# Optimization experiments

Measured on AMD Instinct MI355X. Metric: run time of the kernel, lower is better.

Reference implementation:

```python
import jax, jax.numpy as jnp
import numpy as np

B, S, NB = 8, 512, 23
INIT, E, R, T = 512, 256, 3, 2
NEG = -9e8

def _gru(x, h, wih, whh, bih, bhh):
    gi = x @ wih.T + bih
    gh = h @ whh.T + bhh
    ir, iz, inn = jnp.split(gi, 3, axis=-1)
    hr, hz, hn = jnp.split(gh, 3, axis=-1)
    r = jax.nn.sigmoid(ir + hr)
    z = jax.nn.sigmoid(iz + hz)
    n = jnp.tanh(inn + r * hn)
    return (1.0 - z) * n + z * h

def setup_inputs():
    key = jax.random.key(0)
    ks = jax.random.split(key, 30)
    def lin(k, o, i):
        return jax.random.normal(k, (o, i), jnp.float32) * 0.02
    def vec(k, n):
        return jax.random.normal(k, (n,), jnp.float32) * 0.02
    inp = {}
    inp["amino_list"] = jax.random.normal(ks[0], (B, S, INIT), jnp.float32)
    inp["amino_mask"] = (jax.random.uniform(ks[1], (B, S)) < 0.9).astype(jnp.float32)
    inp["emb_W"] = lin(ks[2], E, INIT); inp["emb_b"] = vec(ks[3], E)
    inp["nb_W"] = lin(ks[4], E, INIT); inp["nb_b"] = vec(ks[5], E)
    inp["align_W"] = jax.random.normal(ks[6], (R, 1, 2 * E), jnp.float32) * 0.02
    inp["align_b"] = jax.random.normal(ks[7], (R, 1), jnp.float32) * 0.02
    inp["attend_W"] = jax.random.normal(ks[8], (R, E, E), jnp.float32) * 0.02
    inp["attend_b"] = jax.random.normal(ks[9], (R, E), jnp.float32) * 0.02
    inp["gru_wih"] = jax.random.normal(ks[10], (R, 3 * E, E), jnp.float32) * 0.02
    inp["gru_whh"] = jax.random.normal(ks[11], (R, 3 * E, E), jnp.float32) * 0.02
    inp["gru_bih"] = jax.random.normal(ks[12], (R, 3 * E), jnp.float32) * 0.02
    inp["gru_bhh"] = jax.random.normal(ks[13], (R, 3 * E), jnp.float32) * 0.02
    inp["seq_align_W"] = lin(ks[14], 1, 2 * E); inp["seq_align_b"] = vec(ks[15], 1)
    inp["seq_attend_W"] = lin(ks[16], E, E); inp["seq_attend_b"] = vec(ks[17], E)
    inp["seq_gru_wih"] = lin(ks[18], 3 * E, E); inp["seq_gru_bih"] = vec(ks[19], 3 * E)
    inp["seq_gru_whh"] = lin(ks[20], 3 * E, E); inp["seq_gru_bhh"] = vec(ks[21], 3 * E)
    inp["amino_degree_list"] = jax.random.randint(ks[22], (B, S, NB), -1, S)
    return inp

def reference(amino_list, amino_mask, emb_W, emb_b, nb_W, nb_b, align_W, align_b,
              attend_W, attend_b, gru_wih, gru_whh, gru_bih, gru_bhh,
              seq_align_W, seq_align_b, seq_attend_W, seq_attend_b,
              seq_gru_wih, seq_gru_whh, seq_gru_bih, seq_gru_bhh, amino_degree_list):
    idx = amino_degree_list
    lrelu = jax.nn.leaky_relu
    # per-batch neighbor gather: (S,D),(S,NB) -> (S,NB,D); index -1 wraps (masked out below)
    gather = jax.vmap(lambda f, i: f[i])
    feat = lrelu(amino_list @ emb_W.T + emb_b)               # (B,S,E)
    nfeat = lrelu(gather(amino_list, idx) @ nb_W.T + nb_b)   # (B,S,NB,E)
    attend_mask = (idx != -1).astype(feat.dtype)             # (B,S,NB)
    smask = jnp.where(idx == -1, NEG, 0.0).astype(feat.dtype)

    def attn(d, center, nbr):
        # align Linear on concat([center, nbr]) split into two matvecs (same math, no concat)
        aW = align_W[d, 0]
        score = lrelu(jnp.einsum('bse,e->bs', center, aW[:E])[:, :, None]
                      + jnp.einsum('bsne,e->bsn', nbr, aW[E:]) + align_b[d, 0])
        w = jax.nn.softmax(score + smask, axis=-1) * attend_mask   # softmax over neighbor axis
        nt = nbr @ attend_W[d].T + attend_b[d]
        return jax.nn.elu(jnp.einsum('bsn,bsne->bse', w, nt))

    h = _gru(attn(0, feat, nfeat).reshape(-1, E), feat.reshape(-1, E),
             gru_wih[0], gru_whh[0], gru_bih[0], gru_bhh[0])
    act = jax.nn.relu(h.reshape(B, S, E))
    for d in range(1, R):
        ctx = attn(d, act, gather(act, idx))
        h = _gru(ctx.reshape(-1, E), h, gru_wih[d], gru_whh[d], gru_bih[d], gru_bhh[d])
        act = jax.nn.relu(h.reshape(B, S, E))

    seq_feature = jnp.sum(act * amino_mask[:, :, None], axis=1)  # (B,E)
    act_mol = jax.nn.relu(seq_feature)                           # fixed across T (as in torch)
    seq_smask = jnp.where(amino_mask == 0, NEG, 0.0)
    saW = seq_align_W[0]
    act_seq = act_mol
    for _ in range(T):
        score = lrelu((act_mol @ saW[:E])[:, None]
                      + jnp.einsum('bse,e->bs', act, saW[E:]) + seq_align_b[0])
        w = jax.nn.softmax(score + seq_smask, axis=-1) * amino_mask  # softmax over seq axis
        tf = act @ seq_attend_W.T + seq_attend_b
        seq_ctx = jax.nn.elu(jnp.einsum('bs,bse->be', w, tf))
        seq_feature = _gru(seq_ctx, seq_feature, seq_gru_wih, seq_gru_whh, seq_gru_bih, seq_gru_bhh)
        act_seq = jax.nn.relu(seq_feature)
    return (act_seq, act)
```

## Files before the change

### kernel.cpp

```cpp
#include <hip/hip_runtime.h>
#include <math.h>


#define BSZ   8
#define SEQ   512
#define NBR   23
#define EMB   256
#define INITD 512
#define BS    (BSZ*SEQ)
#define G3    (3*EMB)
#define NEGV  -9e8f

typedef __attribute__((ext_vector_type(8))) short short8;
typedef __attribute__((ext_vector_type(4))) float f32x4;

__device__ __forceinline__ float lrelu(float x){ return x > 0.f ? x : 0.01f*x; }
__device__ __forceinline__ float elu1 (float x){ return x > 0.f ? x : (expf(x)-1.f); }
__device__ __forceinline__ float sigm (float x){ return 1.f/(1.f+expf(-x)); }
__device__ __forceinline__ float bf2f(ushort u){
    union { unsigned int i; float f; } v; v.i = ((unsigned int)u) << 16; return v.f;
}
__device__ __forceinline__ ushort f2bf(float f){
    union { float f; unsigned int i; } v; v.f = f;
    unsigned int u = v.i;
    return (ushort)((u + 0x7FFFu + ((u >> 16) & 1u)) >> 16);
}

__device__ __forceinline__ void gload_lds16(const void* g, void* l) {
    __builtin_amdgcn_global_load_lds(
        (const __attribute__((address_space(1))) unsigned int*)g,
        (__attribute__((address_space(3))) unsigned int*)l,
        16, 0, 0);
}

template<int BN> struct GemmLdsT {
    ushort A[2][128][64];
    ushort B[2][BN][64];
};

__global__ __launch_bounds__(256) void convert9_kernel(
    const float* s0, ushort* d0, int n0,
    const float* s1, ushort* d1, int n1,
    const float* s2, ushort* d2, int n2,
    const float* s3, ushort* d3, int n3,
    const float* s4, ushort* d4, int n4,
    const float* s5, ushort* d5, int n5,
    const float* s6, ushort* d6, int n6,
    const float* s7, ushort* d7, int n7,
    const float* s8, ushort* d8, int n8)
{
    const float* srcs[9] = {s0,s1,s2,s3,s4,s5,s6,s7,s8};
    ushort* dsts[9] = {d0,d1,d2,d3,d4,d5,d6,d7,d8};
    int ns[9] = {n0,n1,n2,n3,n4,n5,n6,n7,n8};
    int seg = blockIdx.y;
    const float* s = srcs[seg]; ushort* d = dsts[seg]; int n = ns[seg];
    size_t i = ((size_t)blockIdx.x * 256 + threadIdx.x) * 8;
    size_t stride = (size_t)gridDim.x * 256 * 8;
    for (; i < (size_t)n; i += stride) {
        float4 a = *reinterpret_cast<const float4*>(s + i);
        float4 b = *reinterpret_cast<const float4*>(s + i + 4);
        uint4 o;
        o.x = (unsigned)f2bf(a.x) | ((unsigned)f2bf(a.y) << 16);
        o.y = (unsigned)f2bf(a.z) | ((unsigned)f2bf(a.w) << 16);
        o.z = (unsigned)f2bf(b.x) | ((unsigned)f2bf(b.y) << 16);
        o.w = (unsigned)f2bf(b.z) | ((unsigned)f2bf(b.w) << 16);
        *reinterpret_cast<uint4*>(d + i) = o;
    }
}

template<int BN, int ACT, bool WF32, bool WBF>
__device__ __forceinline__ void gemm_dev(
    const ushort* __restrict__ A, const ushort* __restrict__ W,
    const float* __restrict__ bias,
    float* __restrict__ C, ushort* __restrict__ Cbf,
    int N, int K, int bx, int by, GemmLdsT<BN>& L)
{
    constexpr int FN = BN / 32;
    const int tid = threadIdx.x;
    const int m0 = bx * 128, n0 = by * BN;
    const int wv = tid >> 6, lane = tid & 63;
    const int fr = lane & 15, grp = lane >> 4;
    const int kc = K >> 3;
    const int mh = wv & 1, nh = wv >> 1;
    const int lrow = lane >> 3;
    const int csrc = (lane & 7) ^ lrow;

    f32x4 acc[4][FN];
    #pragma unroll
    for (int i = 0; i < 4; ++i)
        #pragma unroll
        for (int n = 0; n < FN; ++n) acc[i][n] = (f32x4){0.f,0.f,0.f,0.f};

    auto stage = [&](int c, int k0) {
        const int kch = (k0 >> 3) + csrc;
        #pragma unroll
        for (int i = 0; i < 4; ++i) {
            const int s = (wv << 2) + i;
            const ushort* g = A + ((size_t)(m0 + (s << 3) + lrow) * kc + kch) * 8;
            gload_lds16(g, &L.A[c][s << 3][0]);
        }
        #pragma unroll
        for (int i = 0; i < FN; ++i) {
            const int s = wv * FN + i;
            const ushort* g = W + ((size_t)(n0 + (s << 3) + lrow) * kc + kch) * 8;
            gload_lds16(g, &L.B[c][s << 3][0]);
        }
    };

    auto compute = [&](int c) {
        #pragma unroll
        for (int ks = 0; ks < 2; ++ks) {
            short8 af[4];
            #pragma unroll
            for (int i = 0; i < 4; ++i) {
                const int ar = (mh << 6) + (i << 4) + fr;
                af[i] = *reinterpret_cast<const short8*>(
                    &L.A[c][ar][(((ks << 2) + grp) ^ (ar & 7)) << 3]);
            }
            #pragma unroll
            for (int n = 0; n < FN; ++n) {
                const int br = nh * (BN/2) + (n << 4) + fr;
                short8 bv = *reinterpret_cast<const short8*>(
                    &L.B[c][br][(((ks << 2) + grp) ^ (br & 7)) << 3]);
                #pragma unroll
                for (int i = 0; i < 4; ++i)
                    acc[i][n] = __builtin_amdgcn_mfma_f32_16x16x32_bf16(
                        af[i], bv, acc[i][n], 0, 0, 0);
            }
        }
    };

    const int KT = K >> 6;
    stage(0, 0);
    __syncthreads();
    int cur = 0;
    for (int kt = 1; kt < KT; ++kt) {
        stage(cur ^ 1, kt << 6);
        compute(cur);
        __syncthreads();
        cur ^= 1;
    }
    compute(cur);

    #pragma unroll
    for (int i = 0; i < 4; ++i) {
        const int mrow = m0 + (mh << 6) + (i << 4) + (grp << 2);
        #pragma unroll
        for (int n = 0; n < FN; ++n) {
            const int col = n0 + nh * (BN/2) + (n << 4) + fr;
            const float bv = bias[col];
            #pragma unroll
            for (int j = 0; j < 4; ++j) {
                float t = acc[i][n][j] + bv;
                if (ACT == 1) t = lrelu(t);
                size_t off = (size_t)(mrow + j) * N + col;
                if (WF32) C[off] = t;
                if (WBF)  Cbf[off] = f2bf(t);
            }
        }
    }
}

template<int ACT, bool WF32, bool WBF>
__global__ __launch_bounds__(256) void gemm_mfma128(
    const ushort* __restrict__ A, const ushort* __restrict__ W,
    const float* __restrict__ bias,
    float* __restrict__ C, ushort* __restrict__ Cbf, int N, int K)
{
    __shared__ GemmLdsT<128> L;
    gemm_dev<128,ACT,WF32,WBF>(A, W, bias, C, Cbf, N, K,
                               blockIdx.x & 31, blockIdx.x >> 5, L);
}

__global__ __launch_bounds__(256) void featnbase_kernel(
    const ushort* __restrict__ aminobf,
    const ushort* __restrict__ embWbf, const float* __restrict__ embB,
    float* __restrict__ feat, ushort* __restrict__ featbf,
    const ushort* __restrict__ nbWbf, const float* __restrict__ nbB,
    float* __restrict__ nbase, ushort* __restrict__ nbasebf)
{
    __shared__ GemmLdsT<64> L;
    int blk = blockIdx.x;
    if (blk < 128)
        gemm_dev<64,1,true,true>(aminobf, embWbf, embB, feat, featbf,
                                 EMB, INITD, blk & 31, blk >> 5, L);
    else {
        blk -= 128;
        gemm_dev<64,1,true,true>(aminobf, nbWbf, nbB, nbase, nbasebf,
                                 EMB, INITD, blk & 31, blk >> 5, L);
    }
}

__global__ __launch_bounds__(256) void round_pre_kernel(
    const ushort* __restrict__ nbrbf, const ushort* __restrict__ attWd,
    const float* __restrict__ attBd, ushort* __restrict__ ntb,
    const ushort* __restrict__ hprevbf, const ushort* __restrict__ gwhhd,
    const float* __restrict__ gbhhd, ushort* __restrict__ ghbf,
    const float* __restrict__ center, const float* __restrict__ nbrbase,
    const float* __restrict__ alignWd,
    float* __restrict__ cdot, float* __restrict__ ndot)
{
    __shared__ GemmLdsT<128> L;
    int blk = blockIdx.x;
    if (blk < 64) {
        gemm_dev<128,0,false,true>(nbrbf, attWd, attBd, nullptr, ntb,
                                   EMB, EMB, blk & 31, blk >> 5, L);
    } else if (blk < 256) {
        int b = blk - 64;
        gemm_dev<128,0,false,true>(hprevbf, gwhhd, gbhhd, nullptr, ghbf,
                                   G3, EMB, b & 31, b >> 5, L);
    } else {
        const int b    = blk - 256;
        const int lane = threadIdx.x & 63;
        const int wv   = threadIdx.x >> 6;
        const int e    = lane << 2;
        const int rb   = b * 32 + wv * 8;
        float4 w0 = *reinterpret_cast<const float4*>(&alignWd[e]);
        float4 w1 = *reinterpret_cast<const float4*>(&alignWd[EMB + e]);
        #pragma unroll
        for (int i = 0; i < 8; ++i) {
            const int r = rb + i;
            float4 xc = *reinterpret_cast<const float4*>(&center[(size_t)r*EMB + e]);
            float4 xn = *reinterpret_cast<const float4*>(&nbrbase[(size_t)r*EMB + e]);
            float ac = xc.x*w0.x + xc.y*w0.y + xc.z*w0.z + xc.w*w0.w;
            float an = xn.x*w1.x + xn.y*w1.y + xn.z*w1.z + xn.w*w1.w;
            #pragma unroll
            for (int off = 32; off; off >>= 1) {
                ac += __shfl_xor(ac, off, 64);
                an += __shfl_xor(an, off, 64);
            }
            if (lane == 0) { cdot[r] = ac; ndot[r] = an; }
        }
    }
}

__global__ __launch_bounds__(256) void attn_kernel(
    const float* __restrict__ cdot, const float* __restrict__ ndot,
    const int* __restrict__ idx, const ushort* __restrict__ nt,
    const float* __restrict__ alignB, ushort* __restrict__ ctxbf)
{
    const int lane = threadIdx.x & 63;
    const int r = blockIdx.x * 4 + (threadIdx.x >> 6);
    const int b = r >> 9;
    float sc = -3e38f, vm = 0.f; int row = 0;
    if (lane < NBR) {
        int j = idx[(size_t)r*NBR + lane];
        int valid = (j >= 0);
        int jj = valid ? j : j + SEQ;
        row = b*SEQ + jj;
        vm = (float)valid;
        sc = lrelu(cdot[r] + ndot[row] + alignB[0]) + (valid ? 0.f : NEGV);
    }
    float m = sc;
    #pragma unroll
    for (int off = 32; off; off >>= 1) m = fmaxf(m, __shfl_xor(m, off, 64));
    float ev = (lane < NBR) ? expf(sc - m) : 0.f;
    float s = ev;
    #pragma unroll
    for (int off = 32; off; off >>= 1) s += __shfl_xor(s, off, 64);
    float wgt = ev * vm / s;
    float acc0 = 0.f, acc1 = 0.f, acc2 = 0.f, acc3 = 0.f;
    const int e = lane << 2;
    #pragma unroll 1
    for (int n = 0; n < NBR; ++n) {
        float wn = __shfl(wgt, n, 64);
        int   rn = __shfl(row, n, 64);
        ushort4 v = *reinterpret_cast<const ushort4*>(&nt[(size_t)rn*EMB + e]);
        acc0 += wn * bf2f(v.x); acc1 += wn * bf2f(v.y);
        acc2 += wn * bf2f(v.z); acc3 += wn * bf2f(v.w);
    }
    uint2 o;
    o.x = (unsigned)f2bf(elu1(acc0)) | ((unsigned)f2bf(elu1(acc1)) << 16);
    o.y = (unsigned)f2bf(elu1(acc2)) | ((unsigned)f2bf(elu1(acc3)) << 16);
    *reinterpret_cast<uint2*>(&ctxbf[(size_t)r*EMB + e]) = o;
}

__global__ __launch_bounds__(256) void gru_kernel(
    const ushort* __restrict__ gibf, const ushort* __restrict__ ghbf,
    const float* __restrict__ hprev,
    float* __restrict__ hout, ushort* __restrict__ hbf,
    float* __restrict__ actout, ushort* __restrict__ actbf)
{
    const size_t r = blockIdx.x * 4 + (threadIdx.x >> 6);
    const int    e = (threadIdx.x & 63) << 2;
    const size_t gb = r*G3 + e, hb = r*EMB + e;
    ushort4 ir4 = *reinterpret_cast<const ushort4*>(&gibf[gb]);
    ushort4 iz4 = *reinterpret_cast<const ushort4*>(&gibf[gb + EMB]);
    ushort4 in4 = *reinterpret_cast<const ushort4*>(&gibf[gb + 2*EMB]);
    ushort4 hr4 = *reinterpret_cast<const ushort4*>(&ghbf[gb]);
    ushort4 hz4 = *reinterpret_cast<const ushort4*>(&ghbf[gb + EMB]);
    ushort4 hn4 = *reinterpret_cast<const ushort4*>(&ghbf[gb + 2*EMB]);
    float4 hp4 = *reinterpret_cast<const float4*>(&hprev[hb]);
    const float ir_[4] = {bf2f(ir4.x),bf2f(ir4.y),bf2f(ir4.z),bf2f(ir4.w)};
    const float iz_[4] = {bf2f(iz4.x),bf2f(iz4.y),bf2f(iz4.z),bf2f(iz4.w)};
    const float in_[4] = {bf2f(in4.x),bf2f(in4.y),bf2f(in4.z),bf2f(in4.w)};
    const float hr_[4] = {bf2f(hr4.x),bf2f(hr4.y),bf2f(hr4.z),bf2f(hr4.w)};
    const float hz_[4] = {bf2f(hz4.x),bf2f(hz4.y),bf2f(hz4.z),bf2f(hz4.w)};
    const float hn_[4] = {bf2f(hn4.x),bf2f(hn4.y),bf2f(hn4.z),bf2f(hn4.w)};
    const float hp_[4] = {hp4.x,hp4.y,hp4.z,hp4.w};
    float hv[4], av[4];
    #pragma unroll
    for (int i = 0; i < 4; ++i) {
        float rg = sigm(ir_[i] + hr_[i]);
        float z  = sigm(iz_[i] + hz_[i]);
        float n  = tanhf(in_[i] + rg*hn_[i]);
        hv[i] = (1.f - z)*n + z*hp_[i];
        av[i] = fmaxf(hv[i], 0.f);
    }
    *reinterpret_cast<float4*>(&hout[hb])   = make_float4(hv[0],hv[1],hv[2],hv[3]);
    *reinterpret_cast<float4*>(&actout[hb]) = make_float4(av[0],av[1],av[2],av[3]);
    uint2 hp, ap;
    hp.x = (unsigned)f2bf(hv[0]) | ((unsigned)f2bf(hv[1]) << 16);
    hp.y = (unsigned)f2bf(hv[2]) | ((unsigned)f2bf(hv[3]) << 16);
    ap.x = (unsigned)f2bf(av[0]) | ((unsigned)f2bf(av[1]) << 16);
    ap.y = (unsigned)f2bf(av[2]) | ((unsigned)f2bf(av[3]) << 16);
    *reinterpret_cast<uint2*>(&hbf[hb])   = hp;
    *reinterpret_cast<uint2*>(&actbf[hb]) = ap;
}

__global__ __launch_bounds__(256) void seqpre_kernel(
    const ushort* __restrict__ actbf, const ushort* __restrict__ satWbf,
    const float* __restrict__ satB, float* __restrict__ tf,
    const float* __restrict__ act, const float* __restrict__ mask,
    const float* __restrict__ saW,
    float* __restrict__ seqfeat, float* __restrict__ cmol,
    float* __restrict__ ad)
{
    __shared__ GemmLdsT<64> L;
    int blk = blockIdx.x;
    if (blk < 128) {
        gemm_dev<64,0,true,false>(actbf, satWbf, satB, tf, nullptr,
                                  EMB, EMB, blk & 31, blk >> 5, L);
    } else if (blk < 136) {
        const int b = blk - 128;
        const int e = threadIdx.x;
        float acc = 0.f;
        for (int s = 0; s < SEQ; ++s)
            acc += act[((size_t)b*SEQ + s)*EMB + e] * mask[b*SEQ + s];
        seqfeat[b*EMB + e] = acc;
        float* red = reinterpret_cast<float*>(&L);
        red[e] = fmaxf(acc, 0.f) * saW[e];
        __syncthreads();
        for (int off = 128; off; off >>= 1) {
            if (e < off) red[e] += red[e + off];
            __syncthreads();
        }
        if (e == 0) cmol[b] = red[0];
    } else {
        const int b2   = blk - 136;
        const int lane = threadIdx.x & 63;
        const int wv   = threadIdx.x >> 6;
        const int e    = lane << 2;
        const int rb   = b2 * 32 + wv * 8;
        float4 w1 = *reinterpret_cast<const float4*>(&saW[EMB + e]);
        #pragma unroll
        for (int i = 0; i < 8; ++i) {
            const int r = rb + i;
            float4 xa = *reinterpret_cast<const float4*>(&act[(size_t)r*EMB + e]);
            float an = xa.x*w1.x + xa.y*w1.y + xa.z*w1.z + xa.w*w1.w;
            #pragma unroll
            for (int off = 32; off; off >>= 1) an += __shfl_xor(an, off, 64);
            if (lane == 0) ad[r] = an;
        }
    }
}

__global__ __launch_bounds__(256) void seqpv2_kernel(
    const float* __restrict__ ad, const float* __restrict__ mask,
    const float* __restrict__ saB, const float* __restrict__ cmol,
    const float* __restrict__ tf, float* __restrict__ partial)
{
    const int st = blockIdx.x, b = blockIdx.y;
    const int tid = threadIdx.x;
    __shared__ float w_s[SEQ];
    __shared__ float red[256];
    float mk0 = mask[b*SEQ + tid], mk1 = mask[b*SEQ + 256 + tid];
    float cb = cmol[b], bb = saB[0];
    float s0 = lrelu(cb + ad[b*SEQ + tid] + bb)       + (mk0 == 0.f ? NEGV : 0.f);
    float s1 = lrelu(cb + ad[b*SEQ + 256 + tid] + bb) + (mk1 == 0.f ? NEGV : 0.f);
    red[tid] = fmaxf(s0, s1); __syncthreads();
    for (int off = 128; off; off >>= 1) {
        if (tid < off) red[tid] = fmaxf(red[tid], red[tid + off]);
        __syncthreads();
    }
    float m = red[0]; __syncthreads();
    float e0 = expf(s0 - m), e1 = expf(s1 - m);
    red[tid] = e0 + e1; __syncthreads();
    for (int off = 128; off; off >>= 1) {
        if (tid < off) red[tid] += red[tid + off];
        __syncthreads();
    }
    float inv = 1.f / red[0];
    w_s[tid]       = e0 * inv * mk0;
    w_s[tid + 256] = e1 * inv * mk1;
    __syncthreads();
    float acc = 0.f;
    const int s0i = st * 32;
    #pragma unroll 4
    for (int s = s0i; s < s0i + 32; ++s)
        acc += w_s[s] * tf[((size_t)b*SEQ + s)*EMB + tid];
    partial[((size_t)b*16 + st)*EMB + tid] = acc;
}

template<int T0>
__global__ __launch_bounds__(512) void seqstep_kernel(
    const float* __restrict__ partial, const float* __restrict__ sfin,
    const ushort* __restrict__ sgwihbf, const float* __restrict__ sgbih,
    const ushort* __restrict__ sgwhhbf, const float* __restrict__ sgbhh,
    float* __restrict__ sgi, float* __restrict__ sfout,
    float* __restrict__ actseq)
{
    const int b = blockIdx.x >> 2, q = blockIdx.x & 3;
    const int tid = threadIdx.x, lane = tid & 63, wv = tid >> 6;
    __shared__ float xs[EMB];
    __shared__ float hs[EMB];
    __shared__ float gis[192], ghs[192];
    if (tid < EMB) {
        hs[tid] = sfin[b*EMB + tid];
        if (T0) {
            float a = 0.f;
            #pragma unroll
            for (int st = 0; st < 16; ++st)
                a += partial[((size_t)b*16 + st)*EMB + tid];
            xs[tid] = elu1(a);
        }
    }
    if (!T0) {
        for (int l = tid; l < 192; l += 512) {
            int g = (l >> 6)*EMB + (q << 6) + (l & 63);
            gis[l] = sgi[b*G3 + g];
        }
    }
    __syncthreads();
    const int nrows = T0 ? 384 : 192;
    const int rpw = nrows >> 3;
    for (int i = 0; i < rpw; ++i) {
        const int l = wv * rpw + i;
        const int iswih = T0 && (l < 192);
        const int ll = (T0 && l >= 192) ? l - 192 : l;
        const int g = (ll >> 6)*EMB + (q << 6) + (ll & 63);
        const ushort* Wm = iswih ? sgwihbf : sgwhhbf;
        ushort4 w4 = *reinterpret_cast<const ushort4*>(&Wm[(size_t)g*EMB + (lane << 2)]);
        float4 x4 = *reinterpret_cast<const float4*>(iswih ? &xs[lane << 2] : &hs[lane << 2]);
        float d = bf2f(w4.x)*x4.x + bf2f(w4.y)*x4.y + bf2f(w4.z)*x4.z + bf2f(w4.w)*x4.w;
        #pragma unroll
        for (int off = 32; off; off >>= 1) d += __shfl_xor(d, off, 64);
        if (lane == 0) {
            if (iswih) {
                d += sgbih[g];
                gis[ll] = d;
                sgi[b*G3 + g] = d;
            } else {
                ghs[ll] = d + sgbhh[g];
            }
        }
    }
    __syncthreads();
    if (tid < 64) {
        const int e = (q << 6) + tid;
        float rg = sigm(gis[tid]       + ghs[tid]);
        float z  = sigm(gis[64 + tid]  + ghs[64 + tid]);
        float n  = tanhf(gis[128 + tid] + rg*ghs[128 + tid]);
        float hv = (1.f - z)*n + z*hs[e];
        sfout[b*EMB + e]  = hv;
        actseq[b*EMB + e] = fmaxf(hv, 0.f);
    }
}

extern "C" void kernel_launch(void* const* d_in, const int* in_sizes, int n_in,
                              void* d_out, int out_size, void* d_ws, size_t ws_size,
                              hipStream_t stream) {
    (void)in_sizes; (void)n_in; (void)out_size; (void)ws_size;
    const float* amino  = (const float*)d_in[0];
    const float* mask   = (const float*)d_in[1];
    const float* embW   = (const float*)d_in[2];
    const float* embB   = (const float*)d_in[3];
    const float* nbW    = (const float*)d_in[4];
    const float* nbB    = (const float*)d_in[5];
    const float* alignW = (const float*)d_in[6];
    const float* alignB = (const float*)d_in[7];
    const float* attW   = (const float*)d_in[8];
    const float* attB   = (const float*)d_in[9];
    const float* gwih   = (const float*)d_in[10];
    const float* gwhh   = (const float*)d_in[11];
    const float* gbih   = (const float*)d_in[12];
    const float* gbhh   = (const float*)d_in[13];
    const float* saW    = (const float*)d_in[14];
    const float* saB    = (const float*)d_in[15];
    const float* satW   = (const float*)d_in[16];
    const float* satB   = (const float*)d_in[17];
    const float* sgwih  = (const float*)d_in[18];
    const float* sgbih  = (const float*)d_in[19];
    const float* sgwhh  = (const float*)d_in[20];
    const float* sgbhh  = (const float*)d_in[21];
    const int*   idx    = (const int*)d_in[22];

    char* cur = (char*)d_ws;
    auto alloc = [&](size_t bytes) -> char* {
        char* p = cur; cur += (bytes + 255) & ~(size_t)255; return p;
    };
    float* feat    = (float*)alloc((size_t)BS*EMB*4);
    float* nbase   = (float*)alloc((size_t)BS*EMB*4);
    float* h       = (float*)alloc((size_t)BS*EMB*4);
    float* tf      = (float*)alloc((size_t)BS*EMB*4);
    float* cdot    = (float*)alloc(BS*4);
    float* ndot    = (float*)alloc(BS*4);
    float* ad      = (float*)alloc(BS*4);
    float* seqfeat = (float*)alloc(BSZ*EMB*4);
    float* sf2     = (float*)alloc(BSZ*EMB*4);
    float* cmol    = (float*)alloc(64*4);
    float* sgi     = (float*)alloc(BSZ*G3*4);
    float* partial = (float*)alloc((size_t)BSZ*16*EMB*4);
    ushort* aminobf = (ushort*)alloc((size_t)BS*INITD*2);
    ushort* featbf  = (ushort*)alloc((size_t)BS*EMB*2);
    ushort* nbasebf = (ushort*)alloc((size_t)BS*EMB*2);
    ushort* actbf   = (ushort*)alloc((size_t)BS*EMB*2);
    ushort* hbf     = (ushort*)alloc((size_t)BS*EMB*2);
    ushort* ctxbf   = (ushort*)alloc((size_t)BS*EMB*2);
    ushort* ntb     = (ushort*)alloc((size_t)BS*EMB*2);
    ushort* gibf    = (ushort*)alloc((size_t)BS*G3*2);
    ushort* ghbf    = (ushort*)alloc((size_t)BS*G3*2);
    ushort* embWbf  = (ushort*)alloc((size_t)EMB*INITD*2);
    ushort* nbWbf   = (ushort*)alloc((size_t)EMB*INITD*2);
    ushort* attWbf  = (ushort*)alloc((size_t)3*EMB*EMB*2);
    ushort* gwihbf  = (ushort*)alloc((size_t)3*G3*EMB*2);
    ushort* gwhhbf  = (ushort*)alloc((size_t)3*G3*EMB*2);
    ushort* satWbf  = (ushort*)alloc((size_t)EMB*EMB*2);
    ushort* sgwihbf = (ushort*)alloc((size_t)G3*EMB*2);
    ushort* sgwhhbf = (ushort*)alloc((size_t)G3*EMB*2);

    float* out    = (float*)d_out;
    float* actseq = out;
    float* act    = out + BSZ*EMB;

    convert9_kernel<<<dim3(1024, 9), 256, 0, stream>>>(
        amino, aminobf, BS*INITD,
        embW,  embWbf,  EMB*INITD,
        nbW,   nbWbf,   EMB*INITD,
        attW,  attWbf,  3*EMB*EMB,
        gwih,  gwihbf,  3*G3*EMB,
        gwhh,  gwhhbf,  3*G3*EMB,
        satW,  satWbf,  EMB*EMB,
        sgwih, sgwihbf, G3*EMB,
        sgwhh, sgwhhbf, G3*EMB);

    featnbase_kernel<<<256, 256, 0, stream>>>(
        aminobf, embWbf, embB, feat, featbf, nbWbf, nbB, nbase, nbasebf);

    for (int d = 0; d < 3; ++d) {
        const float*  center   = (d == 0) ? feat    : act;
        const float*  nbrbase  = (d == 0) ? nbase   : act;
        const ushort* nbrbf    = (d == 0) ? nbasebf : actbf;
        const float*  hprev    = (d == 0) ? feat    : h;
        const ushort* hprevbf  = (d == 0) ? featbf  : hbf;
        round_pre_kernel<<<384, 256, 0, stream>>>(
            nbrbf, attWbf + (size_t)d*EMB*EMB, attB + d*EMB, ntb,
            hprevbf, gwhhbf + (size_t)d*G3*EMB, gbhh + d*G3, ghbf,
            center, nbrbase, alignW + d*2*EMB, cdot, ndot);
        attn_kernel<<<BS/4, 256, 0, stream>>>(cdot, ndot, idx, ntb, alignB + d, ctxbf);
        gemm_mfma128<0,false,true><<<192, 256, 0, stream>>>(
            ctxbf, gwihbf + (size_t)d*G3*EMB, gbih + d*G3, nullptr, gibf, G3, EMB);
        gru_kernel<<<BS/4, 256, 0, stream>>>(gibf, ghbf, hprev, h, hbf, act, actbf);
    }

    seqpre_kernel<<<264, 256, 0, stream>>>(
        actbf, satWbf, satB, tf, act, mask, saW, seqfeat, cmol, ad);
    seqpv2_kernel<<<dim3(16, BSZ), 256, 0, stream>>>(ad, mask, saB, cmol, tf, partial);
    seqstep_kernel<1><<<32, 512, 0, stream>>>(
        partial, seqfeat, sgwihbf, sgbih, sgwhhbf, sgbhh, sgi, sf2, actseq);
    seqstep_kernel<0><<<32, 512, 0, stream>>>(
        partial, sf2, sgwihbf, sgbih, sgwhhbf, sgbhh, sgi, seqfeat, actseq);
}
```

Before: 191.0 us.

## Reorder attention as gather-then-project and fuse attend, GRU GEMMs and gating per round

Each round now gathers and softmax-weights the raw neighbour features first, then applies the attend projection to the aggregated context. Because the weights sum to wsum, the attend bias becomes wsum times the bias. A single fused kernel then runs, per 16-row tile, the attend GEMM with elu, both GRU GEMMs, the gate math, and the next round's alignment dot products. This removes separate GEMM launches and the round trips of the gi, gh and neighbour-transform intermediates through global memory. The two sequence GRU steps collapse into one per-batch tail kernel. The cost is that weights are read straight from global memory without LDS staging, tiles are small, and bf16 rounding of the pre-projection context may change numerics.

```diff
diff --git a/kernel.cpp b/kernel.cpp
--- a/kernel.cpp
+++ b/kernel.cpp
@@ -32,11 +32,6 @@
         (__attribute__((address_space(3))) unsigned int*)l,
         16, 0, 0);
 }
-
-template<int BN> struct GemmLdsT {
-    ushort A[2][128][64];
-    ushort B[2][BN][64];
-};
 
 __global__ __launch_bounds__(256) void convert9_kernel(
     const float* s0, ushort* d0, int n0,
@@ -68,16 +63,17 @@
     }
 }
 
-template<int BN, int ACT, bool WF32, bool WBF>
-__device__ __forceinline__ void gemm_dev(
+struct GemmLds64 { ushort A[2][128][64]; ushort B[2][64][64]; };
+
+template<int ACT>
+__device__ __forceinline__ void gemm64_dev(
     const ushort* __restrict__ A, const ushort* __restrict__ W,
     const float* __restrict__ bias,
     float* __restrict__ C, ushort* __restrict__ Cbf,
-    int N, int K, int bx, int by, GemmLdsT<BN>& L)
-{
-    constexpr int FN = BN / 32;
+    int N, int K, int bx, int by, GemmLds64& L)
+{
     const int tid = threadIdx.x;
-    const int m0 = bx * 128, n0 = by * BN;
+    const int m0 = bx * 128, n0 = by * 64;
     const int wv = tid >> 6, lane = tid & 63;
     const int fr = lane & 15, grp = lane >> 4;
     const int kc = K >> 3;
@@ -85,28 +81,27 @@
     const int lrow = lane >> 3;
     const int csrc = (lane & 7) ^ lrow;
 
-    f32x4 acc[4][FN];
+    f32x4 acc[4][2];
     #pragma unroll
     for (int i = 0; i < 4; ++i)
         #pragma unroll
-        for (int n = 0; n < FN; ++n) acc[i][n] = (f32x4){0.f,0.f,0.f,0.f};
+        for (int n = 0; n < 2; ++n) acc[i][n] = (f32x4){0.f,0.f,0.f,0.f};
 
     auto stage = [&](int c, int k0) {
         const int kch = (k0 >> 3) + csrc;
         #pragma unroll
         for (int i = 0; i < 4; ++i) {
             const int s = (wv << 2) + i;
-            const ushort* g = A + ((size_t)(m0 + (s << 3) + lrow) * kc + kch) * 8;
-            gload_lds16(g, &L.A[c][s << 3][0]);
-        }
-        #pragma unroll
-        for (int i = 0; i < FN; ++i) {
-            const int s = wv * FN + i;
-            const ushort* g = W + ((size_t)(n0 + (s << 3) + lrow) * kc + kch) * 8;
-            gload_lds16(g, &L.B[c][s << 3][0]);
+            gload_lds16(A + ((size_t)(m0 + (s << 3) + lrow) * kc + kch) * 8,
+                        &L.A[c][s << 3][0]);
+        }
+        #pragma unroll
+        for (int i = 0; i < 2; ++i) {
+            const int s = (wv << 1) + i;
+            gload_lds16(W + ((size_t)(n0 + (s << 3) + lrow) * kc + kch) * 8,
+                        &L.B[c][s << 3][0]);
         }
     };
-
     auto compute = [&](int c) {
         #pragma unroll
         for (int ks = 0; ks < 2; ++ks) {
@@ -118,8 +113,8 @@
                     &L.A[c][ar][(((ks << 2) + grp) ^ (ar & 7)) << 3]);
             }
             #pragma unroll
-            for (int n = 0; n < FN; ++n) {
-                const int br = nh * (BN/2) + (n << 4) + fr;
+            for (int n = 0; n < 2; ++n) {
+                const int br = (nh << 5) + (n << 4) + fr;
                 short8 bv = *reinterpret_cast<const short8*>(
                     &L.B[c][br][(((ks << 2) + grp) ^ (br & 7)) << 3]);
                 #pragma unroll
@@ -146,30 +141,19 @@
     for (int i = 0; i < 4; ++i) {
         const int mrow = m0 + (mh << 6) + (i << 4) + (grp << 2);
         #pragma unroll
-        for (int n = 0; n < FN; ++n) {
-            const int col = n0 + nh * (BN/2) + (n << 4) + fr;
+        for (int n = 0; n < 2; ++n) {
+            const int col = n0 + (nh << 5) + (n << 4) + fr;
             const float bv = bias[col];
             #pragma unroll
             for (int j = 0; j < 4; ++j) {
                 float t = acc[i][n][j] + bv;
                 if (ACT == 1) t = lrelu(t);
                 size_t off = (size_t)(mrow + j) * N + col;
-                if (WF32) C[off] = t;
-                if (WBF)  Cbf[off] = f2bf(t);
+                if (C)   C[off] = t;
+                if (Cbf) Cbf[off] = f2bf(t);
             }
         }
     }
-}
-
-template<int ACT, bool WF32, bool WBF>
-__global__ __launch_bounds__(256) void gemm_mfma128(
-    const ushort* __restrict__ A, const ushort* __restrict__ W,
-    const float* __restrict__ bias,
-    float* __restrict__ C, ushort* __restrict__ Cbf, int N, int K)
-{
-    __shared__ GemmLdsT<128> L;
-    gemm_dev<128,ACT,WF32,WBF>(A, W, bias, C, Cbf, N, K,
-                               blockIdx.x & 31, blockIdx.x >> 5, L);
 }
 
 __global__ __launch_bounds__(256) void featnbase_kernel(
@@ -179,65 +163,48 @@
     const ushort* __restrict__ nbWbf, const float* __restrict__ nbB,
     float* __restrict__ nbase, ushort* __restrict__ nbasebf)
 {
-    __shared__ GemmLdsT<64> L;
+    __shared__ GemmLds64 L;
     int blk = blockIdx.x;
     if (blk < 128)
-        gemm_dev<64,1,true,true>(aminobf, embWbf, embB, feat, featbf,
-                                 EMB, INITD, blk & 31, blk >> 5, L);
+        gemm64_dev<1>(aminobf, embWbf, embB, feat, featbf, EMB, INITD, blk & 31, blk >> 5, L);
     else {
         blk -= 128;
-        gemm_dev<64,1,true,true>(aminobf, nbWbf, nbB, nbase, nbasebf,
-                                 EMB, INITD, blk & 31, blk >> 5, L);
-    }
-}
-
-__global__ __launch_bounds__(256) void round_pre_kernel(
-    const ushort* __restrict__ nbrbf, const ushort* __restrict__ attWd,
-    const float* __restrict__ attBd, ushort* __restrict__ ntb,
-    const ushort* __restrict__ hprevbf, const ushort* __restrict__ gwhhd,
-    const float* __restrict__ gbhhd, ushort* __restrict__ ghbf,
+        gemm64_dev<1>(aminobf, nbWbf, nbB, nbase, nbasebf, EMB, INITD, blk & 31, blk >> 5, L);
+    }
+}
+
+__global__ __launch_bounds__(256) void dot2_kernel(
     const float* __restrict__ center, const float* __restrict__ nbrbase,
     const float* __restrict__ alignWd,
     float* __restrict__ cdot, float* __restrict__ ndot)
 {
-    __shared__ GemmLdsT<128> L;
-    int blk = blockIdx.x;
-    if (blk < 64) {
-        gemm_dev<128,0,false,true>(nbrbf, attWd, attBd, nullptr, ntb,
-                                   EMB, EMB, blk & 31, blk >> 5, L);
-    } else if (blk < 256) {
-        int b = blk - 64;
-        gemm_dev<128,0,false,true>(hprevbf, gwhhd, gbhhd, nullptr, ghbf,
-                                   G3, EMB, b & 31, b >> 5, L);
-    } else {
-        const int b    = blk - 256;
-        const int lane = threadIdx.x & 63;
-        const int wv   = threadIdx.x >> 6;
-        const int e    = lane << 2;
-        const int rb   = b * 32 + wv * 8;
-        float4 w0 = *reinterpret_cast<const float4*>(&alignWd[e]);
-        float4 w1 = *reinterpret_cast<const float4*>(&alignWd[EMB + e]);
-        #pragma unroll
-        for (int i = 0; i < 8; ++i) {
-            const int r = rb + i;
-            float4 xc = *reinterpret_cast<const float4*>(&center[(size_t)r*EMB + e]);
-            float4 xn = *reinterpret_cast<const float4*>(&nbrbase[(size_t)r*EMB + e]);
-            float ac = xc.x*w0.x + xc.y*w0.y + xc.z*w0.z + xc.w*w0.w;
-            float an = xn.x*w1.x + xn.y*w1.y + xn.z*w1.z + xn.w*w1.w;
-            #pragma unroll
-            for (int off = 32; off; off >>= 1) {
-                ac += __shfl_xor(ac, off, 64);
-                an += __shfl_xor(an, off, 64);
-            }
-            if (lane == 0) { cdot[r] = ac; ndot[r] = an; }
-        }
-    }
-}
-
-__global__ __launch_bounds__(256) void attn_kernel(
+    const int lane = threadIdx.x & 63;
+    const int wv   = threadIdx.x >> 6;
+    const int e    = lane << 2;
+    const int rb   = blockIdx.x * 32 + wv * 8;
+    float4 w0 = *reinterpret_cast<const float4*>(&alignWd[e]);
+    float4 w1 = *reinterpret_cast<const float4*>(&alignWd[EMB + e]);
+    #pragma unroll
+    for (int i = 0; i < 8; ++i) {
+        const int r = rb + i;
+        float4 xc = *reinterpret_cast<const float4*>(&center[(size_t)r*EMB + e]);
+        float4 xn = *reinterpret_cast<const float4*>(&nbrbase[(size_t)r*EMB + e]);
+        float ac = xc.x*w0.x + xc.y*w0.y + xc.z*w0.z + xc.w*w0.w;
+        float an = xn.x*w1.x + xn.y*w1.y + xn.z*w1.z + xn.w*w1.w;
+        #pragma unroll
+        for (int off = 32; off; off >>= 1) {
+            ac += __shfl_xor(ac, off, 64);
+            an += __shfl_xor(an, off, 64);
+        }
+        if (lane == 0) { cdot[r] = ac; ndot[r] = an; }
+    }
+}
+
+__global__ __launch_bounds__(256) void gather_kernel(
     const float* __restrict__ cdot, const float* __restrict__ ndot,
-    const int* __restrict__ idx, const ushort* __restrict__ nt,
-    const float* __restrict__ alignB, ushort* __restrict__ ctxbf)
+    const int* __restrict__ idx, const ushort* __restrict__ nbr,
+    const float* __restrict__ alignBd,
+    ushort* __restrict__ ctxprebf, float* __restrict__ wsum)
 {
     const int lane = threadIdx.x & 63;
     const int r = blockIdx.x * 4 + (threadIdx.x >> 6);
@@ -249,7 +216,7 @@
         int jj = valid ? j : j + SEQ;
         row = b*SEQ + jj;
         vm = (float)valid;
-        sc = lrelu(cdot[r] + ndot[row] + alignB[0]) + (valid ? 0.f : NEGV);
+        sc = lrelu(cdot[r] + ndot[row] + alignBd[0]) + (valid ? 0.f : NEGV);
     }
     float m = sc;
     #pragma unroll
@@ -259,63 +226,210 @@
     #pragma unroll
     for (int off = 32; off; off >>= 1) s += __shfl_xor(s, off, 64);
     float wgt = ev * vm / s;
+    float ws = wgt;
+    #pragma unroll
+    for (int off = 32; off; off >>= 1) ws += __shfl_xor(ws, off, 64);
     float acc0 = 0.f, acc1 = 0.f, acc2 = 0.f, acc3 = 0.f;
     const int e = lane << 2;
     #pragma unroll 1
     for (int n = 0; n < NBR; ++n) {
         float wn = __shfl(wgt, n, 64);
         int   rn = __shfl(row, n, 64);
-        ushort4 v = *reinterpret_cast<const ushort4*>(&nt[(size_t)rn*EMB + e]);
+        ushort4 v = *reinterpret_cast<const ushort4*>(&nbr[(size_t)rn*EMB + e]);
         acc0 += wn * bf2f(v.x); acc1 += wn * bf2f(v.y);
         acc2 += wn * bf2f(v.z); acc3 += wn * bf2f(v.w);
     }
     uint2 o;
-    o.x = (unsigned)f2bf(elu1(acc0)) | ((unsigned)f2bf(elu1(acc1)) << 16);
-    o.y = (unsigned)f2bf(elu1(acc2)) | ((unsigned)f2bf(elu1(acc3)) << 16);
-    *reinterpret_cast<uint2*>(&ctxbf[(size_t)r*EMB + e]) = o;
-}
-
-__global__ __launch_bounds__(256) void gru_kernel(
-    const ushort* __restrict__ gibf, const ushort* __restrict__ ghbf,
-    const float* __restrict__ hprev,
+    o.x = (unsigned)f2bf(acc0) | ((unsigned)f2bf(acc1) << 16);
+    o.y = (unsigned)f2bf(acc2) | ((unsigned)f2bf(acc3) << 16);
+    *reinterpret_cast<uint2*>(&ctxprebf[(size_t)r*EMB + e]) = o;
+    if (lane == 0) wsum[r] = ws;
+}
+
+struct DLds {
+    ushort ctxpre[16][256];
+    ushort ctx[16][256];
+    ushort hpv[16][256];
+    ushort gis[16][768];
+    ushort ghs[16][768];
+    float  wsum_s[16];
+};
+
+__device__ __forceinline__ void unpack8(uint4 v, float* o) {
+    o[0]=bf2f((ushort)(v.x&0xffff)); o[1]=bf2f((ushort)(v.x>>16));
+    o[2]=bf2f((ushort)(v.y&0xffff)); o[3]=bf2f((ushort)(v.y>>16));
+    o[4]=bf2f((ushort)(v.z&0xffff)); o[5]=bf2f((ushort)(v.z>>16));
+    o[6]=bf2f((ushort)(v.w&0xffff)); o[7]=bf2f((ushort)(v.w>>16));
+}
+
+template<int LAST>
+__global__ __launch_bounds__(512, 4) void fusedD_kernel(
+    const ushort* __restrict__ ctxprebf, const float* __restrict__ wsum,
+    const ushort* __restrict__ attWd, const float* __restrict__ attBd,
+    const ushort* __restrict__ gwihd, const float* __restrict__ gbihd,
+    const ushort* __restrict__ gwhhd, const float* __restrict__ gbhhd,
+    const float* __restrict__ hprev, const ushort* __restrict__ hprevbf,
+    const float* __restrict__ nextW,
     float* __restrict__ hout, ushort* __restrict__ hbf,
-    float* __restrict__ actout, ushort* __restrict__ actbf)
-{
-    const size_t r = blockIdx.x * 4 + (threadIdx.x >> 6);
-    const int    e = (threadIdx.x & 63) << 2;
-    const size_t gb = r*G3 + e, hb = r*EMB + e;
-    ushort4 ir4 = *reinterpret_cast<const ushort4*>(&gibf[gb]);
-    ushort4 iz4 = *reinterpret_cast<const ushort4*>(&gibf[gb + EMB]);
-    ushort4 in4 = *reinterpret_cast<const ushort4*>(&gibf[gb + 2*EMB]);
-    ushort4 hr4 = *reinterpret_cast<const ushort4*>(&ghbf[gb]);
-    ushort4 hz4 = *reinterpret_cast<const ushort4*>(&ghbf[gb + EMB]);
-    ushort4 hn4 = *reinterpret_cast<const ushort4*>(&ghbf[gb + 2*EMB]);
-    float4 hp4 = *reinterpret_cast<const float4*>(&hprev[hb]);
-    const float ir_[4] = {bf2f(ir4.x),bf2f(ir4.y),bf2f(ir4.z),bf2f(ir4.w)};
-    const float iz_[4] = {bf2f(iz4.x),bf2f(iz4.y),bf2f(iz4.z),bf2f(iz4.w)};
-    const float in_[4] = {bf2f(in4.x),bf2f(in4.y),bf2f(in4.z),bf2f(in4.w)};
-    const float hr_[4] = {bf2f(hr4.x),bf2f(hr4.y),bf2f(hr4.z),bf2f(hr4.w)};
-    const float hz_[4] = {bf2f(hz4.x),bf2f(hz4.y),bf2f(hz4.z),bf2f(hz4.w)};
-    const float hn_[4] = {bf2f(hn4.x),bf2f(hn4.y),bf2f(hn4.z),bf2f(hn4.w)};
-    const float hp_[4] = {hp4.x,hp4.y,hp4.z,hp4.w};
-    float hv[4], av[4];
-    #pragma unroll
-    for (int i = 0; i < 4; ++i) {
-        float rg = sigm(ir_[i] + hr_[i]);
-        float z  = sigm(iz_[i] + hz_[i]);
-        float n  = tanhf(in_[i] + rg*hn_[i]);
-        hv[i] = (1.f - z)*n + z*hp_[i];
-        av[i] = fmaxf(hv[i], 0.f);
-    }
-    *reinterpret_cast<float4*>(&hout[hb])   = make_float4(hv[0],hv[1],hv[2],hv[3]);
-    *reinterpret_cast<float4*>(&actout[hb]) = make_float4(av[0],av[1],av[2],av[3]);
-    uint2 hp, ap;
-    hp.x = (unsigned)f2bf(hv[0]) | ((unsigned)f2bf(hv[1]) << 16);
-    hp.y = (unsigned)f2bf(hv[2]) | ((unsigned)f2bf(hv[3]) << 16);
-    ap.x = (unsigned)f2bf(av[0]) | ((unsigned)f2bf(av[1]) << 16);
-    ap.y = (unsigned)f2bf(av[2]) | ((unsigned)f2bf(av[3]) << 16);
-    *reinterpret_cast<uint2*>(&hbf[hb])   = hp;
-    *reinterpret_cast<uint2*>(&actbf[hb]) = ap;
+    float* __restrict__ actout, ushort* __restrict__ actbf,
+    float* __restrict__ cdotO, float* __restrict__ ndotO)
+{
+    __shared__ DLds L;
+    const int tid = threadIdx.x;
+    const int r0 = blockIdx.x * 16;
+
+    {
+        const int ri = tid >> 5, c = tid & 31;
+        uint4 v = *reinterpret_cast<const uint4*>(&ctxprebf[(size_t)(r0+ri)*EMB + (c<<3)]);
+        *reinterpret_cast<uint4*>(&L.ctxpre[ri][(c ^ (ri&7)) << 3]) = v;
+        uint4 h = *reinterpret_cast<const uint4*>(&hprevbf[(size_t)(r0+ri)*EMB + (c<<3)]);
+        *reinterpret_cast<uint4*>(&L.hpv[ri][(c ^ (ri&7)) << 3]) = h;
+        if (tid < 16) L.wsum_s[tid] = wsum[r0 + tid];
+    }
+    __syncthreads();
+
+    const int wv = tid >> 6, lane = tid & 63;
+    const int fr = lane & 15, grp = lane >> 4;
+
+    {
+        f32x4 acc[2] = {(f32x4){0,0,0,0},(f32x4){0,0,0,0}};
+        #pragma unroll
+        for (int kt = 0; kt < 8; ++kt) {
+            short8 af = *reinterpret_cast<const short8*>(
+                &L.ctxpre[fr][((((kt<<2)+grp) ^ (fr&7)) << 3)]);
+            #pragma unroll
+            for (int f = 0; f < 2; ++f) {
+                const int col = (wv<<5) + (f<<4) + fr;
+                short8 bv = *reinterpret_cast<const short8*>(
+                    &attWd[(size_t)col*EMB + (kt<<5) + (grp<<3)]);
+                acc[f] = __builtin_amdgcn_mfma_f32_16x16x32_bf16(af, bv, acc[f], 0, 0, 0);
+            }
+        }
+        #pragma unroll
+        for (int f = 0; f < 2; ++f) {
+            const int col = (wv<<5) + (f<<4) + fr;
+            const float bb = attBd[col];
+            const int ch = col >> 3;
+            #pragma unroll
+            for (int j = 0; j < 4; ++j) {
+                const int row = (grp<<2) + j;
+                float t = elu1(acc[f][j] + L.wsum_s[row]*bb);
+                L.ctx[row][(((ch ^ (row&7)) << 3) | (col & 7))] = f2bf(t);
+            }
+        }
+    }
+    __syncthreads();
+
+    {
+        f32x4 acc[6];
+        #pragma unroll
+        for (int f = 0; f < 6; ++f) acc[f] = (f32x4){0,0,0,0};
+        #pragma unroll
+        for (int kt = 0; kt < 8; ++kt) {
+            short8 af = *reinterpret_cast<const short8*>(
+                &L.ctx[fr][((((kt<<2)+grp) ^ (fr&7)) << 3)]);
+            #pragma unroll
+            for (int f = 0; f < 6; ++f) {
+                const int col = wv*96 + (f<<4) + fr;
+                short8 bv = *reinterpret_cast<const short8*>(
+                    &gwihd[(size_t)col*EMB + (kt<<5) + (grp<<3)]);
+                acc[f] = __builtin_amdgcn_mfma_f32_16x16x32_bf16(af, bv, acc[f], 0, 0, 0);
+            }
+        }
+        #pragma unroll
+        for (int f = 0; f < 6; ++f) {
+            const int col = wv*96 + (f<<4) + fr;
+            const float bb = gbihd[col];
+            #pragma unroll
+            for (int j = 0; j < 4; ++j)
+                L.gis[(grp<<2)+j][col] = f2bf(acc[f][j] + bb);
+        }
+        #pragma unroll
+        for (int f = 0; f < 6; ++f) acc[f] = (f32x4){0,0,0,0};
+        #pragma unroll
+        for (int kt = 0; kt < 8; ++kt) {
+            short8 af = *reinterpret_cast<const short8*>(
+                &L.hpv[fr][((((kt<<2)+grp) ^ (fr&7)) << 3)]);
+            #pragma unroll
+            for (int f = 0; f < 6; ++f) {
+                const int col = wv*96 + (f<<4) + fr;
+                short8 bv = *reinterpret_cast<const short8*>(
+                    &gwhhd[(size_t)col*EMB + (kt<<5) + (grp<<3)]);
+                acc[f] = __builtin_amdgcn_mfma_f32_16x16x32_bf16(af, bv, acc[f], 0, 0, 0);
+            }
+        }
+        #pragma unroll
+        for (int f = 0; f < 6; ++f) {
+            const int col = wv*96 + (f<<4) + fr;
+            const float bb = gbhhd[col];
+            #pragma unroll
+            for (int j = 0; j < 4; ++j)
+                L.ghs[(grp<<2)+j][col] = f2bf(acc[f][j] + bb);
+        }
+    }
+    __syncthreads();
+
+    {
+        const int row = tid >> 5, sub = tid & 31;
+        const int e0 = sub << 3;
+        const size_t r = (size_t)r0 + row;
+        uint4 giA = *reinterpret_cast<const uint4*>(&L.gis[row][e0]);
+        uint4 giB = *reinterpret_cast<const uint4*>(&L.gis[row][256 + e0]);
+        uint4 giC = *reinterpret_cast<const uint4*>(&L.gis[row][512 + e0]);
+        uint4 ghA = *reinterpret_cast<const uint4*>(&L.ghs[row][e0]);
+        uint4 ghB = *reinterpret_cast<const uint4*>(&L.ghs[row][256 + e0]);
+        uint4 ghC = *reinterpret_cast<const uint4*>(&L.ghs[row][512 + e0]);
+        float4 hp0 = *reinterpret_cast<const float4*>(&hprev[r*EMB + e0]);
+        float4 hp1 = *reinterpret_cast<const float4*>(&hprev[r*EMB + e0 + 4]);
+        float ir_[8], iz_[8], in_[8], hr_[8], hz_[8], hn_[8];
+        unpack8(giA, ir_); unpack8(giB, iz_); unpack8(giC, in_);
+        unpack8(ghA, hr_); unpack8(ghB, hz_); unpack8(ghC, hn_);
+        const float hp_[8] = {hp0.x,hp0.y,hp0.z,hp0.w,hp1.x,hp1.y,hp1.z,hp1.w};
+        float hv8[8], av8[8];
+        #pragma unroll
+        for (int i = 0; i < 8; ++i) {
+            float rg = sigm(ir_[i] + hr_[i]);
+            float z  = sigm(iz_[i] + hz_[i]);
+            float n  = tanhf(in_[i] + rg*hn_[i]);
+            hv8[i] = (1.f - z)*n + z*hp_[i];
+            av8[i] = fmaxf(hv8[i], 0.f);
+        }
+        *reinterpret_cast<float4*>(&hout[r*EMB + e0])       = make_float4(hv8[0],hv8[1],hv8[2],hv8[3]);
+        *reinterpret_cast<float4*>(&hout[r*EMB + e0 + 4])   = make_float4(hv8[4],hv8[5],hv8[6],hv8[7]);
+        *reinterpret_cast<float4*>(&actout[r*EMB + e0])     = make_float4(av8[0],av8[1],av8[2],av8[3]);
+        *reinterpret_cast<float4*>(&actout[r*EMB + e0 + 4]) = make_float4(av8[4],av8[5],av8[6],av8[7]);
+        uint4 hb, ab;
+        hb.x = (unsigned)f2bf(hv8[0]) | ((unsigned)f2bf(hv8[1]) << 16);
+        hb.y = (unsigned)f2bf(hv8[2]) | ((unsigned)f2bf(hv8[3]) << 16);
+        hb.z = (unsigned)f2bf(hv8[4]) | ((unsigned)f2bf(hv8[5]) << 16);
+        hb.w = (unsigned)f2bf(hv8[6]) | ((unsigned)f2bf(hv8[7]) << 16);
+        ab.x = (unsigned)f2bf(av8[0]) | ((unsigned)f2bf(av8[1]) << 16);
+        ab.y = (unsigned)f2bf(av8[2]) | ((unsigned)f2bf(av8[3]) << 16);
+        ab.z = (unsigned)f2bf(av8[4]) | ((unsigned)f2bf(av8[5]) << 16);
+        ab.w = (unsigned)f2bf(av8[6]) | ((unsigned)f2bf(av8[7]) << 16);
+        *reinterpret_cast<uint4*>(&hbf[r*EMB + e0])   = hb;
+        *reinterpret_cast<uint4*>(&actbf[r*EMB + e0]) = ab;
+        float pc = 0.f, pn = 0.f;
+        float4 w1a = *reinterpret_cast<const float4*>(&nextW[EMB + e0]);
+        float4 w1b = *reinterpret_cast<const float4*>(&nextW[EMB + e0 + 4]);
+        pn = av8[0]*w1a.x + av8[1]*w1a.y + av8[2]*w1a.z + av8[3]*w1a.w
+           + av8[4]*w1b.x + av8[5]*w1b.y + av8[6]*w1b.z + av8[7]*w1b.w;
+        if (!LAST) {
+            float4 w0a = *reinterpret_cast<const float4*>(&nextW[e0]);
+            float4 w0b = *reinterpret_cast<const float4*>(&nextW[e0 + 4]);
+            pc = av8[0]*w0a.x + av8[1]*w0a.y + av8[2]*w0a.z + av8[3]*w0a.w
+               + av8[4]*w0b.x + av8[5]*w0b.y + av8[6]*w0b.z + av8[7]*w0b.w;
+        }
+        #pragma unroll
+        for (int off = 16; off; off >>= 1) {
+            pn += __shfl_xor(pn, off, 32);
+            if (!LAST) pc += __shfl_xor(pc, off, 32);
+        }
+        if (sub == 0) {
+            if (!LAST) cdotO[r] = pc;
+            ndotO[r] = pn;
+        }
+    }
 }
 
 __global__ __launch_bounds__(256) void seqpre_kernel(
@@ -323,15 +437,13 @@
     const float* __restrict__ satB, float* __restrict__ tf,
     const float* __restrict__ act, const float* __restrict__ mask,
     const float* __restrict__ saW,
-    float* __restrict__ seqfeat, float* __restrict__ cmol,
-    float* __restrict__ ad)
-{
-    __shared__ GemmLdsT<64> L;
+    float* __restrict__ seqfeat, float* __restrict__ cmol)
+{
+    __shared__ GemmLds64 L;
     int blk = blockIdx.x;
     if (blk < 128) {
-        gemm_dev<64,0,true,false>(actbf, satWbf, satB, tf, nullptr,
-                                  EMB, EMB, blk & 31, blk >> 5, L);
-    } else if (blk < 136) {
+        gemm64_dev<0>(actbf, satWbf, satB, tf, nullptr, EMB, EMB, blk & 31, blk >> 5, L);
+    } else {
         const int b = blk - 128;
         const int e = threadIdx.x;
         float acc = 0.f;
@@ -346,22 +458,6 @@
             __syncthreads();
         }
         if (e == 0) cmol[b] = red[0];
-    } else {
-        const int b2   = blk - 136;
-        const int lane = threadIdx.x & 63;
-        const int wv   = threadIdx.x >> 6;
-        const int e    = lane << 2;
-        const int rb   = b2 * 32 + wv * 8;
-        float4 w1 = *reinterpret_cast<const float4*>(&saW[EMB + e]);
-        #pragma unroll
-        for (int i = 0; i < 8; ++i) {
-            const int r = rb + i;
-            float4 xa = *reinterpret_cast<const float4*>(&act[(size_t)r*EMB + e]);
-            float an = xa.x*w1.x + xa.y*w1.y + xa.z*w1.z + xa.w*w1.w;
-            #pragma unroll
-            for (int off = 32; off; off >>= 1) an += __shfl_xor(an, off, 64);
-            if (lane == 0) ad[r] = an;
-        }
     }
 }
 
@@ -402,68 +498,63 @@
     partial[((size_t)b*16 + st)*EMB + tid] = acc;
 }
 
-template<int T0>
-__global__ __launch_bounds__(512) void seqstep_kernel(
-    const float* __restrict__ partial, const float* __restrict__ sfin,
-    const ushort* __restrict__ sgwihbf, const float* __restrict__ sgbih,
-    const ushort* __restrict__ sgwhhbf, const float* __restrict__ sgbhh,
-    float* __restrict__ sgi, float* __restrict__ sfout,
+__global__ __launch_bounds__(512) void seqtail_kernel(
+    const float* __restrict__ partial, const float* __restrict__ seqfeatIn,
+    const ushort* __restrict__ wihbf, const float* __restrict__ bih,
+    const ushort* __restrict__ whhbf, const float* __restrict__ bhh,
     float* __restrict__ actseq)
 {
-    const int b = blockIdx.x >> 2, q = blockIdx.x & 3;
+    const int b = blockIdx.x;
     const int tid = threadIdx.x, lane = tid & 63, wv = tid >> 6;
-    __shared__ float xs[EMB];
-    __shared__ float hs[EMB];
-    __shared__ float gis[192], ghs[192];
+    __shared__ float xs[EMB], hs[EMB], gis[G3], ghs[G3];
     if (tid < EMB) {
-        hs[tid] = sfin[b*EMB + tid];
-        if (T0) {
-            float a = 0.f;
-            #pragma unroll
-            for (int st = 0; st < 16; ++st)
-                a += partial[((size_t)b*16 + st)*EMB + tid];
-            xs[tid] = elu1(a);
-        }
-    }
-    if (!T0) {
-        for (int l = tid; l < 192; l += 512) {
-            int g = (l >> 6)*EMB + (q << 6) + (l & 63);
-            gis[l] = sgi[b*G3 + g];
-        }
-    }
-    __syncthreads();
-    const int nrows = T0 ? 384 : 192;
-    const int rpw = nrows >> 3;
-    for (int i = 0; i < rpw; ++i) {
-        const int l = wv * rpw + i;
-        const int iswih = T0 && (l < 192);
-        const int ll = (T0 && l >= 192) ? l - 192 : l;
-        const int g = (ll >> 6)*EMB + (q << 6) + (ll & 63);
-        const ushort* Wm = iswih ? sgwihbf : sgwhhbf;
-        ushort4 w4 = *reinterpret_cast<const ushort4*>(&Wm[(size_t)g*EMB + (lane << 2)]);
-        float4 x4 = *reinterpret_cast<const float4*>(iswih ? &xs[lane << 2] : &hs[lane << 2]);
-        float d = bf2f(w4.x)*x4.x + bf2f(w4.y)*x4.y + bf2f(w4.z)*x4.z + bf2f(w4.w)*x4.w;
-        #pragma unroll
-        for (int off = 32; off; off >>= 1) d += __shfl_xor(d, off, 64);
-        if (lane == 0) {
-            if (iswih) {
-                d += sgbih[g];
-                gis[ll] = d;
-                sgi[b*G3 + g] = d;
-            } else {
-                ghs[ll] = d + sgbhh[g];
-            }
-        }
-    }
-    __syncthreads();
-    if (tid < 64) {
-        const int e = (q << 6) + tid;
-        float rg = sigm(gis[tid]       + ghs[tid]);
-        float z  = sigm(gis[64 + tid]  + ghs[64 + tid]);
-        float n  = tanhf(gis[128 + tid] + rg*ghs[128 + tid]);
-        float hv = (1.f - z)*n + z*hs[e];
-        sfout[b*EMB + e]  = hv;
-        actseq[b*EMB + e] = fmaxf(hv, 0.f);
+        hs[tid] = seqfeatIn[b*EMB + tid];
+        float a = 0.f;
+        #pragma unroll
+        for (int st = 0; st < 16; ++st)
+            a += partial[((size_t)b*16 + st)*EMB + tid];
+        xs[tid] = elu1(a);
+    }
+    __syncthreads();
+    for (int i = 0; i < 96; ++i) {
+        const int l = wv * 96 + i;
+        ushort4 wi = *reinterpret_cast<const ushort4*>(&wihbf[(size_t)l*EMB + (lane << 2)]);
+        ushort4 wh = *reinterpret_cast<const ushort4*>(&whhbf[(size_t)l*EMB + (lane << 2)]);
+        float4 x4 = *reinterpret_cast<const float4*>(&xs[lane << 2]);
+        float4 h4 = *reinterpret_cast<const float4*>(&hs[lane << 2]);
+        float di = bf2f(wi.x)*x4.x + bf2f(wi.y)*x4.y + bf2f(wi.z)*x4.z + bf2f(wi.w)*x4.w;
+        float dh = bf2f(wh.x)*h4.x + bf2f(wh.y)*h4.y + bf2f(wh.z)*h4.z + bf2f(wh.w)*h4.w;
+        #pragma unroll
+        for (int off = 32; off; off >>= 1) {
+            di += __shfl_xor(di, off, 64);
+            dh += __shfl_xor(dh, off, 64);
+        }
+        if (lane == 0) { gis[l] = di + bih[l]; ghs[l] = dh + bhh[l]; }
+    }
+    __syncthreads();
+    if (tid < EMB) {
+        float rg = sigm(gis[tid] + ghs[tid]);
+        float z  = sigm(gis[EMB + tid] + ghs[EMB + tid]);
+        float n  = tanhf(gis[2*EMB + tid] + rg*ghs[2*EMB + tid]);
+        hs[tid] = (1.f - z)*n + z*hs[tid];
+    }
+    __syncthreads();
+    for (int i = 0; i < 96; ++i) {
+        const int l = wv * 96 + i;
+        ushort4 wh = *reinterpret_cast<const ushort4*>(&whhbf[(size_t)l*EMB + (lane << 2)]);
+        float4 h4 = *reinterpret_cast<const float4*>(&hs[lane << 2]);
+        float dh = bf2f(wh.x)*h4.x + bf2f(wh.y)*h4.y + bf2f(wh.z)*h4.z + bf2f(wh.w)*h4.w;
+        #pragma unroll
+        for (int off = 32; off; off >>= 1) dh += __shfl_xor(dh, off, 64);
+        if (lane == 0) ghs[l] = dh + bhh[l];
+    }
+    __syncthreads();
+    if (tid < EMB) {
+        float rg = sigm(gis[tid] + ghs[tid]);
+        float z  = sigm(gis[EMB + tid] + ghs[EMB + tid]);
+        float n  = tanhf(gis[2*EMB + tid] + rg*ghs[2*EMB + tid]);
+        float hv = (1.f - z)*n + z*hs[tid];
+        actseq[b*EMB + tid] = fmaxf(hv, 0.f);
     }
 }
 
@@ -505,29 +596,24 @@
     float* tf      = (float*)alloc((size_t)BS*EMB*4);
     float* cdot    = (float*)alloc(BS*4);
     float* ndot    = (float*)alloc(BS*4);
-    float* ad      = (float*)alloc(BS*4);
+    float* wsum    = (float*)alloc(BS*4);
     float* seqfeat = (float*)alloc(BSZ*EMB*4);
-    float* sf2     = (float*)alloc(BSZ*EMB*4);
     float* cmol    = (float*)alloc(64*4);
-    float* sgi     = (float*)alloc(BSZ*G3*4);
     float* partial = (float*)alloc((size_t)BSZ*16*EMB*4);
-    ushort* aminobf = (ushort*)alloc((size_t)BS*INITD*2);
-    ushort* featbf  = (ushort*)alloc((size_t)BS*EMB*2);
-    ushort* nbasebf = (ushort*)alloc((size_t)BS*EMB*2);
-    ushort* actbf   = (ushort*)alloc((size_t)BS*EMB*2);
-    ushort* hbf     = (ushort*)alloc((size_t)BS*EMB*2);
-    ushort* ctxbf   = (ushort*)alloc((size_t)BS*EMB*2);
-    ushort* ntb     = (ushort*)alloc((size_t)BS*EMB*2);
-    ushort* gibf    = (ushort*)alloc((size_t)BS*G3*2);
-    ushort* ghbf    = (ushort*)alloc((size_t)BS*G3*2);
-    ushort* embWbf  = (ushort*)alloc((size_t)EMB*INITD*2);
-    ushort* nbWbf   = (ushort*)alloc((size_t)EMB*INITD*2);
-    ushort* attWbf  = (ushort*)alloc((size_t)3*EMB*EMB*2);
-    ushort* gwihbf  = (ushort*)alloc((size_t)3*G3*EMB*2);
-    ushort* gwhhbf  = (ushort*)alloc((size_t)3*G3*EMB*2);
-    ushort* satWbf  = (ushort*)alloc((size_t)EMB*EMB*2);
-    ushort* sgwihbf = (ushort*)alloc((size_t)G3*EMB*2);
-    ushort* sgwhhbf = (ushort*)alloc((size_t)G3*EMB*2);
+    ushort* aminobf  = (ushort*)alloc((size_t)BS*INITD*2);
+    ushort* featbf   = (ushort*)alloc((size_t)BS*EMB*2);
+    ushort* nbasebf  = (ushort*)alloc((size_t)BS*EMB*2);
+    ushort* actbf    = (ushort*)alloc((size_t)BS*EMB*2);
+    ushort* hbf      = (ushort*)alloc((size_t)BS*EMB*2);
+    ushort* ctxprebf = (ushort*)alloc((size_t)BS*EMB*2);
+    ushort* embWbf   = (ushort*)alloc((size_t)EMB*INITD*2);
+    ushort* nbWbf    = (ushort*)alloc((size_t)EMB*INITD*2);
+    ushort* attWbf   = (ushort*)alloc((size_t)3*EMB*EMB*2);
+    ushort* gwihbf   = (ushort*)alloc((size_t)3*G3*EMB*2);
+    ushort* gwhhbf   = (ushort*)alloc((size_t)3*G3*EMB*2);
+    ushort* satWbf   = (ushort*)alloc((size_t)EMB*EMB*2);
+    ushort* sgwihbf  = (ushort*)alloc((size_t)G3*EMB*2);
+    ushort* sgwhhbf  = (ushort*)alloc((size_t)G3*EMB*2);
 
     float* out    = (float*)d_out;
     float* actseq = out;
@@ -547,27 +633,34 @@
     featnbase_kernel<<<256, 256, 0, stream>>>(
         aminobf, embWbf, embB, feat, featbf, nbWbf, nbB, nbase, nbasebf);
 
+    dot2_kernel<<<128, 256, 0, stream>>>(feat, nbase, alignW, cdot, ndot);
+
     for (int d = 0; d < 3; ++d) {
-        const float*  center   = (d == 0) ? feat    : act;
-        const float*  nbrbase  = (d == 0) ? nbase   : act;
-        const ushort* nbrbf    = (d == 0) ? nbasebf : actbf;
-        const float*  hprev    = (d == 0) ? feat    : h;
-        const ushort* hprevbf  = (d == 0) ? featbf  : hbf;
-        round_pre_kernel<<<384, 256, 0, stream>>>(
-            nbrbf, attWbf + (size_t)d*EMB*EMB, attB + d*EMB, ntb,
-            hprevbf, gwhhbf + (size_t)d*G3*EMB, gbhh + d*G3, ghbf,
-            center, nbrbase, alignW + d*2*EMB, cdot, ndot);
-        attn_kernel<<<BS/4, 256, 0, stream>>>(cdot, ndot, idx, ntb, alignB + d, ctxbf);
-        gemm_mfma128<0,false,true><<<192, 256, 0, stream>>>(
-            ctxbf, gwihbf + (size_t)d*G3*EMB, gbih + d*G3, nullptr, gibf, G3, EMB);
-        gru_kernel<<<BS/4, 256, 0, stream>>>(gibf, ghbf, hprev, h, hbf, act, actbf);
-    }
-
-    seqpre_kernel<<<264, 256, 0, stream>>>(
-        actbf, satWbf, satB, tf, act, mask, saW, seqfeat, cmol, ad);
-    seqpv2_kernel<<<dim3(16, BSZ), 256, 0, stream>>>(ad, mask, saB, cmol, tf, partial);
-    seqstep_kernel<1><<<32, 512, 0, stream>>>(
-        partial, seqfeat, sgwihbf, sgbih, sgwhhbf, sgbhh, sgi, sf2, actseq);
-    seqstep_kernel<0><<<32, 512, 0, stream>>>(
-        partial, sf2, sgwihbf, sgbih, sgwhhbf, sgbhh, sgi, seqfeat, actseq);
-}
+        const ushort* nbrbf   = (d == 0) ? nbasebf : actbf;
+        const float*  hprev   = (d == 0) ? feat    : h;
+        const ushort* hprevbf = (d == 0) ? featbf  : hbf;
+        gather_kernel<<<BS/4, 256, 0, stream>>>(
+            cdot, ndot, idx, nbrbf, alignB + d, ctxprebf, wsum);
+        if (d < 2) {
+            fusedD_kernel<0><<<BS/16, 512, 0, stream>>>(
+                ctxprebf, wsum, attWbf + (size_t)d*EMB*EMB, attB + d*EMB,
+                gwihbf + (size_t)d*G3*EMB, gbih + d*G3,
+                gwhhbf + (size_t)d*G3*EMB, gbhh + d*G3,
+                hprev, hprevbf, alignW + (d+1)*2*EMB,
+                h, hbf, act, actbf, cdot, ndot);
+        } else {
+            fusedD_kernel<1><<<BS/16, 512, 0, stream>>>(
+                ctxprebf, wsum, attWbf + (size_t)d*EMB*EMB, attB + d*EMB,
+                gwihbf + (size_t)d*G3*EMB, gbih + d*G3,
+                gwhhbf + (size_t)d*G3*EMB, gbhh + d*G3,
+                hprev, hprevbf, saW,
+                h, hbf, act, actbf, cdot, ndot);
+        }
+    }
+
+    seqpre_kernel<<<136, 256, 0, stream>>>(
+        actbf, satWbf, satB, tf, act, mask, saW, seqfeat, cmol);
+    seqpv2_kernel<<<dim3(16, BSZ), 256, 0, stream>>>(ndot, mask, saB, cmol, tf, partial);
+    seqtail_kernel<<<BSZ, 512, 0, stream>>>(
+        partial, seqfeat, sgwihbf, sgbih, sgwhhbf, sgbhh, actseq);
+}
```

Measured after the change: 321.5 us. 1.68x slower.
